# Kernel optimization log

Hardware: AMD Instinct MI355X
Metric: run time of the kernel (lower is better)

Reference implementation:

```python
import jax, jax.numpy as jnp
import numpy as np

HIDDEN = 1024
NUM_HEADS = 16
HEAD_DIM = HIDDEN // NUM_HEADS
EPS = 1e-05


def setup_inputs() -> dict:
    key = jax.random.key(0)
    ks = jax.random.split(key, 6)
    B, S = 4, 2048
    x = jax.random.normal(ks[0], (B, S, HIDDEN), dtype=jnp.float32)
    # trunc_normal_(std=0.02) approximated by scaled normal
    w_in = jax.random.normal(ks[1], (3 * HIDDEN, HIDDEN), dtype=jnp.float32) * 0.02
    b_in = jax.random.normal(ks[2], (3 * HIDDEN,), dtype=jnp.float32) * 0.02
    w_norm = jnp.ones((HIDDEN,), dtype=jnp.float32)
    lim = 1.0 / np.sqrt(HIDDEN)
    w_out = jax.random.uniform(ks[3], (HIDDEN, HIDDEN), dtype=jnp.float32, minval=-lim, maxval=lim)
    b_out = jax.random.uniform(ks[4], (HIDDEN,), dtype=jnp.float32, minval=-lim, maxval=lim)
    return {"x": x, "w_in": w_in, "b_in": b_in, "w_norm": w_norm, "w_out": w_out, "b_out": b_out}


def _rms_norm(x, w, eps):
    var = jnp.mean(jnp.square(x), axis=-1, keepdims=True)
    return x * jax.lax.rsqrt(var + eps) * w


def reference(x, w_in, b_in, w_norm, w_out, b_out):
    B, S, _ = x.shape
    xn = _rms_norm(x, w_norm, EPS)
    qkv = jnp.einsum('bsd,ed->bse', xn, w_in) + b_in  # [B,S,3*HIDDEN]
    q, k, v = jnp.split(qkv, 3, axis=-1)
    # [B,S,H*D] -> [B,H,S,D]
    def split_heads(t):
        return t.reshape(B, S, NUM_HEADS, HEAD_DIM).transpose(0, 2, 1, 3)
    q, k, v = split_heads(q), split_heads(k), split_heads(v)
    scale = 1.0 / np.sqrt(HEAD_DIM)
    scores = jnp.einsum('bhqd,bhkd->bhqk', q, k) * scale
    attn = jax.nn.softmax(scores, axis=-1)
    o = jnp.einsum('bhqk,bhkd->bhqd', attn, v)
    o = o.transpose(0, 2, 1, 3).reshape(B, S, HIDDEN)
    return jnp.einsum('bsd,ed->bse', o, w_out) + b_out
```

## Files before the change

kernel.cpp:

```cpp
#include <hip/hip_runtime.h>
#include <stdint.h>

typedef short bf16x4 __attribute__((ext_vector_type(4)));
typedef short bf16x8 __attribute__((ext_vector_type(8)));
typedef _Float16 f16x8 __attribute__((ext_vector_type(8)));
typedef float f32x4 __attribute__((ext_vector_type(4)));
typedef float f32x16 __attribute__((ext_vector_type(16)));
typedef unsigned int u32x4 __attribute__((ext_vector_type(4)));
typedef unsigned int u32x2 __attribute__((ext_vector_type(2)));

#if __has_builtin(__builtin_amdgcn_exp2f)
#define EXP2 __builtin_amdgcn_exp2f
#else
#define EXP2 exp2f
#endif

__device__ __forceinline__ short f2bf(float f) {
  union { float f; uint32_t u; } v; v.f = f;
  uint32_t r = (v.u + 0x7fffu + ((v.u >> 16) & 1u)) >> 16;
  return (short)(uint16_t)r;
}

__device__ __forceinline__ unsigned cvtpk_bf16(float lo, float hi) {
  unsigned r;
  asm("v_cvt_pk_bf16_f32 %0, %1, %2" : "=v"(r) : "v"(lo), "v"(hi));
  return r;
}

#if __has_builtin(__builtin_amdgcn_permlane32_swap)
__device__ __forceinline__ void plane32_swap(unsigned& a, unsigned& b) {
  u32x2 r = __builtin_amdgcn_permlane32_swap(a, b, false, false);
  a = r[0]; b = r[1];
}
__device__ __forceinline__ float xhalf_max(float x) {
  unsigned xu = __builtin_bit_cast(unsigned, x);
  u32x2 r = __builtin_amdgcn_permlane32_swap(xu, xu, false, false);
  return fmaxf(__builtin_bit_cast(float, r[0]), __builtin_bit_cast(float, r[1]));
}
__device__ __forceinline__ float xhalf_sum(float x) {
  unsigned xu = __builtin_bit_cast(unsigned, x);
  u32x2 r = __builtin_amdgcn_permlane32_swap(xu, xu, false, false);
  return __builtin_bit_cast(float, r[0]) + __builtin_bit_cast(float, r[1]);
}
#else
__device__ __forceinline__ void plane32_swap(unsigned& a, unsigned& b) {
  asm("s_nop 1\n\tv_permlane32_swap_b32 %0, %1" : "+v"(a), "+v"(b));
}
__device__ __forceinline__ float xhalf_max(float x) { return fmaxf(x, __shfl_xor(x, 32, 64)); }
__device__ __forceinline__ float xhalf_sum(float x) { return x + __shfl_xor(x, 32, 64); }
#endif

__device__ __forceinline__ float fmax3(float a, float b, float c) {
  return fmaxf(fmaxf(a, b), c);
}

__device__ __forceinline__ float tmax16(const f32x16& s) {
  float a0 = fmax3(s[0], s[1], s[2]);
  float a1 = fmax3(s[3], s[4], s[5]);
  float a2 = fmax3(s[6], s[7], s[8]);
  float a3 = fmax3(s[9], s[10], s[11]);
  float a4 = fmax3(s[12], s[13], s[14]);
  float b0 = fmax3(a0, a1, s[15]);
  float b1 = fmax3(a2, a3, a4);
  return fmaxf(b0, b1);
}
__device__ __forceinline__ float tsum16(const f32x16& s) {
  float a0 = (s[0] + s[1]) + (s[2] + s[3]);
  float a1 = (s[4] + s[5]) + (s[6] + s[7]);
  float a2 = (s[8] + s[9]) + (s[10] + s[11]);
  float a3 = (s[12] + s[13]) + (s[14] + s[15]);
  return (a0 + a1) + (a2 + a3);
}

__device__ __forceinline__ f32x16 zero16() {
  f32x16 z;
#pragma unroll
  for (int i = 0; i < 16; ++i) z[i] = 0.f;
  return z;
}

__device__ __forceinline__ void gld_lds16(const void* g, void* l) {
  __builtin_amdgcn_global_load_lds(
      (__attribute__((address_space(1))) const void*)g,
      (__attribute__((address_space(3))) void*)l, 16, 0, 0);
}

__global__ __launch_bounds__(256) void k_rmsnorm(const float* __restrict__ x,
                                                 const float* __restrict__ wn,
                                                 short* __restrict__ xn) {
  const int row = blockIdx.x;
  const int t = threadIdx.x;
  const float4 v = reinterpret_cast<const float4*>(x + (size_t)row * 1024)[t];
  float ss = v.x * v.x + v.y * v.y + v.z * v.z + v.w * v.w;
#pragma unroll
  for (int m = 32; m >= 1; m >>= 1) ss += __shfl_xor(ss, m, 64);
  __shared__ float red[4];
  if ((t & 63) == 0) red[t >> 6] = ss;
  __syncthreads();
  const float tot = red[0] + red[1] + red[2] + red[3];
  const float rr = rsqrtf(tot * (1.0f / 1024.0f) + 1e-5f);
  const float4 g = reinterpret_cast<const float4*>(wn)[t];
  bf16x4 o;
  o[0] = f2bf(v.x * rr * g.x);
  o[1] = f2bf(v.y * rr * g.y);
  o[2] = f2bf(v.z * rr * g.z);
  o[3] = f2bf(v.w * rr * g.w);
  reinterpret_cast<bf16x4*>(xn + (size_t)row * 1024)[t] = o;
}

__global__ __launch_bounds__(256) void k_cast_bf(const float* __restrict__ in,
                                                 short* __restrict__ out, int n4) {
  int i = blockIdx.x * 256 + threadIdx.x;
  if (i >= n4) return;
  float4 v = reinterpret_cast<const float4*>(in)[i];
  bf16x4 o;
  o[0] = f2bf(v.x); o[1] = f2bf(v.y); o[2] = f2bf(v.z); o[3] = f2bf(v.w);
  reinterpret_cast<bf16x4*>(out)[i] = o;
}

__global__ __launch_bounds__(256) void k_cast_f16(const float* __restrict__ in,
                                                  _Float16* __restrict__ out, int n4) {
  int i = blockIdx.x * 256 + threadIdx.x;
  if (i >= n4) return;
  float4 v = reinterpret_cast<const float4*>(in)[i];
  _Float16 o[4] = {(_Float16)v.x, (_Float16)v.y, (_Float16)v.z, (_Float16)v.w};
  reinterpret_cast<ulong1*>(out)[i] = *reinterpret_cast<ulong1*>(o);
}

__global__ __launch_bounds__(256) void k_gemm_qkv(const short* __restrict__ A,
                                                  const short* __restrict__ B,
                                                  const float* __restrict__ bias,
                                                  short* __restrict__ qb,
                                                  short* __restrict__ kfrag,
                                                  short* __restrict__ vfrag) {
  __shared__ __align__(16) short As[128 * 32];
  __shared__ __align__(16) short Bs[128 * 32];
  const int t = threadIdx.x;
  const int orig = blockIdx.y * 24 + blockIdx.x;
  const int swz = (orig & 7) * 192 + (orig >> 3);
  const long bn0 = (long)(swz % 24) * 128;
  const long bm0 = (long)(swz / 24) * 128;
  const int w = t >> 6, l = t & 63;
  const int wr = (w >> 1) * 64, wc = (w & 1) * 64;
  const int lm = l & 15, h = l >> 4;
  f32x4 acc[4][4];
#pragma unroll
  for (int i = 0; i < 4; ++i)
#pragma unroll
    for (int j = 0; j < 4; ++j) acc[i][j] = (f32x4){0.f, 0.f, 0.f, 0.f};
  const int srow = t >> 2, scol = (t & 3) * 8;
  const short* Ag = A + (bm0 + srow) * 1024 + scol;
  const short* Bg = B + (bn0 + srow) * 1024 + scol;
  short* AsP = As + t * 8;
  short* BsP = Bs + t * 8;
  for (int kt = 0; kt < 32; ++kt) {
    const int k0 = kt << 5;
    gld_lds16(Ag + k0, AsP);
    gld_lds16(Ag + k0 + 64 * 1024, AsP + 2048);
    gld_lds16(Bg + k0, BsP);
    gld_lds16(Bg + k0 + 64 * 1024, BsP + 2048);
    __syncthreads();
    bf16x8 af[4], bfr[4];
#pragma unroll
    for (int mi = 0; mi < 4; ++mi)
      af[mi] = *reinterpret_cast<const bf16x8*>(As + (wr + mi * 16 + lm) * 32 + h * 8);
#pragma unroll
    for (int ni = 0; ni < 4; ++ni)
      bfr[ni] = *reinterpret_cast<const bf16x8*>(Bs + (wc + ni * 16 + lm) * 32 + h * 8);
    __builtin_amdgcn_s_setprio(1);
#pragma unroll
    for (int mi = 0; mi < 4; ++mi)
#pragma unroll
      for (int ni = 0; ni < 4; ++ni)
        acc[mi][ni] = __builtin_amdgcn_mfma_f32_16x16x32_bf16(af[mi], bfr[ni], acc[mi][ni], 0, 0, 0);
    __builtin_amdgcn_s_setprio(0);
    __syncthreads();
  }
#pragma unroll
  for (int ni = 0; ni < 4; ++ni) {
    const int ncol = (int)bn0 + wc + ni * 16 + lm;
    const float bv = bias[ncol];
    const int which = ncol >> 10;
    const int e = ncol & 1023;
    const int hd = e >> 6, d = e & 63;
#pragma unroll
    for (int mi = 0; mi < 4; ++mi) {
#pragma unroll
      for (int r = 0; r < 4; ++r) {
        const long mrow = bm0 + wr + mi * 16 + h * 4 + r;
        const float val = acc[mi][ni][r] + bv;
        const long bh = (mrow >> 11) * 16 + hd;
        const int seq = (int)(mrow & 2047);
        if (which == 0) {
          const long off = (bh * 2048 + seq) * 64 + d;
          qb[off] = f2bf(val * 0.18033688011112042f);
        } else if (which == 1) {
          const long off = ((bh * 64 + (seq >> 5)) * 4 + (d >> 4)) * 512 +
                           ((seq & 31) | (((d >> 3) & 1) << 5)) * 8 + (d & 7);
          kfrag[off] = f2bf(val);
        } else {
          const long off = (((bh * 64 + (seq >> 5)) * 2 + (d >> 5)) * 2 +
                            ((seq >> 4) & 1)) * 512 +
                           ((d & 31) | (((seq >> 3) & 1) << 5)) * 8 + (seq & 7);
          vfrag[off] = f2bf(val);
        }
      }
    }
  }
}

__global__ __launch_bounds__(256) void k_gemm_out(const _Float16* __restrict__ A,
                                                  const _Float16* __restrict__ B,
                                                  const float* __restrict__ bias,
                                                  float* __restrict__ outp) {
  __shared__ __align__(16) _Float16 As[128 * 32];
  __shared__ __align__(16) _Float16 Bs[128 * 32];
  const int t = threadIdx.x;
  const int orig = blockIdx.y * 8 + blockIdx.x;
  const int swz = (orig & 7) * 64 + (orig >> 3);
  const long bn0 = (long)(swz % 8) * 128;
  const long bm0 = (long)(swz / 8) * 128;
  const int w = t >> 6, l = t & 63;
  const int wr = (w >> 1) * 64, wc = (w & 1) * 64;
  const int lm = l & 15, h = l >> 4;
  f32x4 acc[4][4];
#pragma unroll
  for (int i = 0; i < 4; ++i)
#pragma unroll
    for (int j = 0; j < 4; ++j) acc[i][j] = (f32x4){0.f, 0.f, 0.f, 0.f};
  const int srow = t >> 2, scol = (t & 3) * 8;
  const _Float16* Ag = A + (bm0 + srow) * 1024 + scol;
  const _Float16* Bg = B + (bn0 + srow) * 1024 + scol;
  _Float16* AsP = As + t * 8;
  _Float16* BsP = Bs + t * 8;
  for (int kt = 0; kt < 32; ++kt) {
    const int k0 = kt << 5;
    gld_lds16(Ag + k0, AsP);
    gld_lds16(Ag + k0 + 64 * 1024, AsP + 2048);
    gld_lds16(Bg + k0, BsP);
    gld_lds16(Bg + k0 + 64 * 1024, BsP + 2048);
    __syncthreads();
    f16x8 af[4], bfr[4];
#pragma unroll
    for (int mi = 0; mi < 4; ++mi)
      af[mi] = *reinterpret_cast<const f16x8*>(As + (wr + mi * 16 + lm) * 32 + h * 8);
#pragma unroll
    for (int ni = 0; ni < 4; ++ni)
      bfr[ni] = *reinterpret_cast<const f16x8*>(Bs + (wc + ni * 16 + lm) * 32 + h * 8);
    __builtin_amdgcn_s_setprio(1);
#pragma unroll
    for (int mi = 0; mi < 4; ++mi)
#pragma unroll
      for (int ni = 0; ni < 4; ++ni)
        acc[mi][ni] = __builtin_amdgcn_mfma_f32_16x16x32_f16(af[mi], bfr[ni], acc[mi][ni], 0, 0, 0);
    __builtin_amdgcn_s_setprio(0);
    __syncthreads();
  }
#pragma unroll
  for (int ni = 0; ni < 4; ++ni) {
    const int ncol = (int)bn0 + wc + ni * 16 + lm;
    const float bv = bias[ncol];
#pragma unroll
    for (int mi = 0; mi < 4; ++mi) {
#pragma unroll
      for (int r = 0; r < 4; ++r) {
        const long mrow = bm0 + wr + mi * 16 + h * 4 + r;
        outp[mrow * 1024 + ncol] = acc[mi][ni][r] + bv;
      }
    }
  }
}

__global__ __launch_bounds__(256) void k_attn(const short* __restrict__ q,
                                              const short* __restrict__ kfrag,
                                              const short* __restrict__ vfrag,
                                              _Float16* __restrict__ o) {
  const int orig = blockIdx.y * 8 + blockIdx.x;
  const int work = (orig & 7) * 64 + (orig >> 3);
  const int bh = work >> 3;
  const int qt = work & 7;
  const int t = threadIdx.x;
  const int w = t >> 6, l = t & 63;
  const int lq = l & 31, hh = l >> 5;
  const int qbase = qt * 256 + w * 64;

  bf16x8 qf[2][4];
#pragma unroll
  for (int qh = 0; qh < 2; ++qh) {
    const short* qp = q + ((size_t)(bh * 2048 + qbase + qh * 32 + lq)) * 64 + hh * 8;
#pragma unroll
    for (int db = 0; db < 4; ++db)
      qf[qh][db] = *reinterpret_cast<const bf16x8*>(qp + db * 16);
  }

  const short* kfb = kfrag + (size_t)bh * 64 * 2048 + l * 8;
  const short* vfb = vfrag + (size_t)bh * 64 * 2048 + l * 8;

  f32x16 oa00 = zero16(), oa01 = zero16();
  f32x16 oa10 = zero16(), oa11 = zero16();
  float mr0 = -1e30f, mr1 = -1e30f, lr0 = 0.f, lr1 = 0.f;

  auto LOAD = [&](bf16x8* kf, bf16x8* vf, int kt) {
    const short* kp = kfb + (size_t)kt * 2048;
#pragma unroll
    for (int db = 0; db < 4; ++db)
      kf[db] = *reinterpret_cast<const bf16x8*>(kp + db * 512);
    const short* vp = vfb + (size_t)kt * 2048;
#pragma unroll
    for (int i = 0; i < 4; ++i)
      vf[i] = *reinterpret_cast<const bf16x8*>(vp + i * 512);
  };

  auto COMPUTE = [&](const bf16x8* kf, const bf16x8* vf) {
    f32x16 s0 = zero16(), s1 = zero16();
    __builtin_amdgcn_s_setprio(1);
#pragma unroll
    for (int db = 0; db < 4; ++db) {
      s0 = __builtin_amdgcn_mfma_f32_32x32x16_bf16(kf[db], qf[0][db], s0, 0, 0, 0);
      s1 = __builtin_amdgcn_mfma_f32_32x32x16_bf16(kf[db], qf[1][db], s1, 0, 0, 0);
    }
    __builtin_amdgcn_s_setprio(0);
    float tm0 = xhalf_max(tmax16(s0));
    float tm1 = xhalf_max(tmax16(s1));
    if (!__all((tm0 <= mr0 + 8.f) && (tm1 <= mr1 + 8.f))) {
      const float mn0 = fmaxf(mr0, tm0), mn1 = fmaxf(mr1, tm1);
      const float c0 = EXP2(mr0 - mn0), c1 = EXP2(mr1 - mn1);
      lr0 *= c0; lr1 *= c1;
#pragma unroll
      for (int r = 0; r < 16; ++r) {
        oa00[r] *= c0; oa01[r] *= c0;
        oa10[r] *= c1; oa11[r] *= c1;
      }
      mr0 = mn0; mr1 = mn1;
    }
#pragma unroll
    for (int r = 0; r < 16; ++r) {
      s0[r] = EXP2(s0[r] - mr0);
      s1[r] = EXP2(s1[r] - mr1);
    }
    lr0 += tsum16(s0);
    lr1 += tsum16(s1);
    __builtin_amdgcn_s_setprio(1);
#pragma unroll
    for (int kg = 0; kg < 2; ++kg) {
      const int b0 = kg * 8;
      unsigned p00 = cvtpk_bf16(s0[b0 + 0], s0[b0 + 1]);
      unsigned p01 = cvtpk_bf16(s0[b0 + 2], s0[b0 + 3]);
      unsigned p02 = cvtpk_bf16(s0[b0 + 4], s0[b0 + 5]);
      unsigned p03 = cvtpk_bf16(s0[b0 + 6], s0[b0 + 7]);
      plane32_swap(p00, p02);
      plane32_swap(p01, p03);
      u32x4 pw0 = {p00, p01, p02, p03};
      bf16x8 pf0 = *reinterpret_cast<bf16x8*>(&pw0);
      unsigned p10 = cvtpk_bf16(s1[b0 + 0], s1[b0 + 1]);
      unsigned p11 = cvtpk_bf16(s1[b0 + 2], s1[b0 + 3]);
      unsigned p12 = cvtpk_bf16(s1[b0 + 4], s1[b0 + 5]);
      unsigned p13 = cvtpk_bf16(s1[b0 + 6], s1[b0 + 7]);
      plane32_swap(p10, p12);
      plane32_swap(p11, p13);
      u32x4 pw1 = {p10, p11, p12, p13};
      bf16x8 pf1 = *reinterpret_cast<bf16x8*>(&pw1);
      oa00 = __builtin_amdgcn_mfma_f32_32x32x16_bf16(vf[0 * 2 + kg], pf0, oa00, 0, 0, 0);
      oa10 = __builtin_amdgcn_mfma_f32_32x32x16_bf16(vf[0 * 2 + kg], pf1, oa10, 0, 0, 0);
      oa01 = __builtin_amdgcn_mfma_f32_32x32x16_bf16(vf[1 * 2 + kg], pf0, oa01, 0, 0, 0);
      oa11 = __builtin_amdgcn_mfma_f32_32x32x16_bf16(vf[1 * 2 + kg], pf1, oa11, 0, 0, 0);
    }
    __builtin_amdgcn_s_setprio(0);
  };

  bf16x8 kfA[4], vfA[4], kfB[4], vfB[4];
  LOAD(kfA, vfA, 0);
  for (int kt = 0; kt < 64; kt += 2) {
    LOAD(kfB, vfB, kt + 1);
    COMPUTE(kfA, vfA);
    int k2 = kt + 2; if (k2 > 63) k2 = 63;
    LOAD(kfA, vfA, k2);
    COMPUTE(kfB, vfB);
  }
  const float inv0 = 1.0f / xhalf_sum(lr0);
  const float inv1 = 1.0f / xhalf_sum(lr1);
  const int b = bh >> 4, hd = bh & 15;
  _Float16* ob0 = o + ((size_t)(b * 2048 + qbase + lq)) * 1024 + hd * 64;
  _Float16* ob1 = ob0 + 32 * 1024;
#pragma unroll
  for (int r2 = 0; r2 < 16; ++r2) {
    const int d0 = (r2 & 3) + 8 * (r2 >> 2) + 4 * hh;
    ob0[d0] = (_Float16)(oa00[r2] * inv0);
    ob0[d0 + 32] = (_Float16)(oa01[r2] * inv0);
    ob1[d0] = (_Float16)(oa10[r2] * inv1);
    ob1[d0 + 32] = (_Float16)(oa11[r2] * inv1);
  }
}

extern "C" void kernel_launch(void* const* d_in, const int* in_sizes, int n_in,
                              void* d_out, int out_size, void* d_ws, size_t ws_size,
                              hipStream_t stream) {
  const float* x = (const float*)d_in[0];
  const float* w_in = (const float*)d_in[1];
  const float* b_in = (const float*)d_in[2];
  const float* w_norm = (const float*)d_in[3];
  const float* w_out = (const float*)d_in[4];
  const float* b_out = (const float*)d_in[5];
  float* out = (float*)d_out;
  char* ws = (char*)d_ws;
  short* xn = (short*)(ws);
  short* win_b = (short*)(ws + 16777216);
  _Float16* wout_h = (_Float16*)(ws + 23068672);
  short* qb = (short*)(ws + 25165824);
  short* kfrag = (short*)(ws + 41943040);
  short* vfrag = (short*)(ws + 58720256);
  _Float16* ob = (_Float16*)(ws + 75497472);

  k_cast_bf<<<3072, 256, 0, stream>>>(w_in, win_b, 786432);
  k_cast_f16<<<1024, 256, 0, stream>>>(w_out, wout_h, 262144);
  k_rmsnorm<<<8192, 256, 0, stream>>>(x, w_norm, xn);
  k_gemm_qkv<<<dim3(24, 64), 256, 0, stream>>>(xn, win_b, b_in, qb, kfrag, vfrag);
  k_attn<<<dim3(8, 64), 256, 0, stream>>>(qb, kfrag, vfrag, ob);
  k_gemm_out<<<dim3(8, 64), 256, 0, stream>>>(ob, wout_h, b_out, out);
}
```

Baseline: 232.6 us.

## Split attention KV range in two halves and merge partial outputs

Splits each attention work item across two blocks that each process half of the key tiles. Each block writes normalized partial outputs plus per-row max and sum statistics, and a new merge kernel combines them with log-sum-exp weights. This doubles the attention grid to raise CU occupancy and parallelism. In exchange it adds an extra kernel launch and about 48MB of extra fp16 read/write traffic for the merge.

```diff
diff --git a/kernel.cpp b/kernel.cpp
--- a/kernel.cpp
+++ b/kernel.cpp
@@ -3,6 +3,7 @@
 
 typedef short bf16x4 __attribute__((ext_vector_type(4)));
 typedef short bf16x8 __attribute__((ext_vector_type(8)));
+typedef _Float16 f16x4 __attribute__((ext_vector_type(4)));
 typedef _Float16 f16x8 __attribute__((ext_vector_type(8)));
 typedef float f32x4 __attribute__((ext_vector_type(4)));
 typedef float f32x16 __attribute__((ext_vector_type(16)));
@@ -274,11 +275,14 @@
 __global__ __launch_bounds__(256) void k_attn(const short* __restrict__ q,
                                               const short* __restrict__ kfrag,
                                               const short* __restrict__ vfrag,
-                                              _Float16* __restrict__ o) {
-  const int orig = blockIdx.y * 8 + blockIdx.x;
-  const int work = (orig & 7) * 64 + (orig >> 3);
-  const int bh = work >> 3;
-  const int qt = work & 7;
+                                              _Float16* __restrict__ po0,
+                                              _Float16* __restrict__ po1,
+                                              float* __restrict__ stats) {
+  const int orig = blockIdx.y * 16 + blockIdx.x;
+  const int work = (orig & 7) * 128 + (orig >> 3);
+  const int bh = work >> 4;
+  const int qt = (work >> 1) & 7;
+  const int half = work & 1;
   const int t = threadIdx.x;
   const int w = t >> 6, l = t & 63;
   const int lq = l & 31, hh = l >> 5;
@@ -369,18 +373,22 @@
   };
 
   bf16x8 kfA[4], vfA[4], kfB[4], vfB[4];
-  LOAD(kfA, vfA, 0);
-  for (int kt = 0; kt < 64; kt += 2) {
+  const int kt0 = half * 32, kt1 = kt0 + 32;
+  LOAD(kfA, vfA, kt0);
+  for (int kt = kt0; kt < kt1; kt += 2) {
     LOAD(kfB, vfB, kt + 1);
     COMPUTE(kfA, vfA);
-    int k2 = kt + 2; if (k2 > 63) k2 = 63;
+    int k2 = kt + 2; if (k2 >= kt1) k2 = kt1 - 1;
     LOAD(kfA, vfA, k2);
     COMPUTE(kfB, vfB);
   }
-  const float inv0 = 1.0f / xhalf_sum(lr0);
-  const float inv1 = 1.0f / xhalf_sum(lr1);
+  const float lt0 = xhalf_sum(lr0);
+  const float lt1 = xhalf_sum(lr1);
+  const float inv0 = 1.0f / lt0;
+  const float inv1 = 1.0f / lt1;
   const int b = bh >> 4, hd = bh & 15;
-  _Float16* ob0 = o + ((size_t)(b * 2048 + qbase + lq)) * 1024 + hd * 64;
+  _Float16* po = half ? po1 : po0;
+  _Float16* ob0 = po + ((size_t)(b * 2048 + qbase + lq)) * 1024 + hd * 64;
   _Float16* ob1 = ob0 + 32 * 1024;
 #pragma unroll
   for (int r2 = 0; r2 < 16; ++r2) {
@@ -390,6 +398,39 @@
     ob1[d0] = (_Float16)(oa10[r2] * inv1);
     ob1[d0 + 32] = (_Float16)(oa11[r2] * inv1);
   }
+  if (hh == 0) {
+    float* st = stats + (size_t)half * 262144;
+    const size_t si = (size_t)bh * 2048 + qbase + lq;
+    st[si] = mr0;
+    st[131072 + si] = lt0;
+    st[si + 32] = mr1;
+    st[131072 + si + 32] = lt1;
+  }
+}
+
+__global__ __launch_bounds__(256) void k_merge(_Float16* __restrict__ po0,
+                                               const _Float16* __restrict__ po1,
+                                               const float* __restrict__ stats) {
+  const int row = blockIdx.x;
+  const int t = threadIdx.x;
+  const int col = t * 4;
+  const int hd = col >> 6;
+  const int b = row >> 11, s = row & 2047;
+  const size_t si = (size_t)(b * 16 + hd) * 2048 + s;
+  const float m0 = stats[si], l0 = stats[131072 + si];
+  const float m1 = stats[262144 + si], l1 = stats[393216 + si];
+  const float mm = fmaxf(m0, m1);
+  const float w0 = l0 * EXP2(m0 - mm), w1 = l1 * EXP2(m1 - mm);
+  const float inv = 1.0f / (w0 + w1);
+  const float a0 = w0 * inv, a1 = w1 * inv;
+  const size_t off = (size_t)row * 1024 + col;
+  f16x4 v0 = *reinterpret_cast<const f16x4*>(po0 + off);
+  f16x4 v1 = *reinterpret_cast<const f16x4*>(po1 + off);
+  f16x4 r;
+#pragma unroll
+  for (int j = 0; j < 4; ++j)
+    r[j] = (_Float16)(a0 * (float)v0[j] + a1 * (float)v1[j]);
+  *reinterpret_cast<f16x4*>(po0 + off) = r;
 }
 
 extern "C" void kernel_launch(void* const* d_in, const int* in_sizes, int n_in,
@@ -404,17 +445,20 @@
   float* out = (float*)d_out;
   char* ws = (char*)d_ws;
   short* xn = (short*)(ws);
+  _Float16* po1 = (_Float16*)(ws);
   short* win_b = (short*)(ws + 16777216);
+  float* stats = (float*)(ws + 16777216);
   _Float16* wout_h = (_Float16*)(ws + 23068672);
   short* qb = (short*)(ws + 25165824);
   short* kfrag = (short*)(ws + 41943040);
   short* vfrag = (short*)(ws + 58720256);
-  _Float16* ob = (_Float16*)(ws + 75497472);
+  _Float16* po0 = (_Float16*)(ws + 75497472);
 
   k_cast_bf<<<3072, 256, 0, stream>>>(w_in, win_b, 786432);
   k_cast_f16<<<1024, 256, 0, stream>>>(w_out, wout_h, 262144);
   k_rmsnorm<<<8192, 256, 0, stream>>>(x, w_norm, xn);
   k_gemm_qkv<<<dim3(24, 64), 256, 0, stream>>>(xn, win_b, b_in, qb, kfrag, vfrag);
-  k_attn<<<dim3(8, 64), 256, 0, stream>>>(qb, kfrag, vfrag, ob);
-  k_gemm_out<<<dim3(8, 64), 256, 0, stream>>>(ob, wout_h, b_out, out);
-}
+  k_attn<<<dim3(16, 64), 256, 0, stream>>>(qb, kfrag, vfrag, po0, po1, stats);
+  k_merge<<<8192, 256, 0, stream>>>(po0, po1, stats);
+  k_gemm_out<<<dim3(8, 64), 256, 0, stream>>>(po0, wout_h, b_out, out);
+}
```

Result: slower. 252.0 us (+8.4%).

## Halve per-wave query rows in attention to raise occupancy

Applied to the files above, without the earlier changes.

Each wave now handles 32 query rows instead of 64, so per-thread accumulators and Q fragments are halved, and the grid doubles to 1024 blocks with launch bounds requesting 4 blocks per CU. V fragments are no longer double-buffered and are loaded just before each compute step. The aim is more waves and better latency hiding. In exchange, K/V are read from global memory twice as often per query row, and each K/V fragment feeds fewer MFMAs.

```diff
diff --git a/kernel.cpp b/kernel.cpp
--- a/kernel.cpp
+++ b/kernel.cpp
@@ -271,40 +271,38 @@
   }
 }
 
-__global__ __launch_bounds__(256) void k_attn(const short* __restrict__ q,
-                                              const short* __restrict__ kfrag,
-                                              const short* __restrict__ vfrag,
-                                              _Float16* __restrict__ o) {
-  const int orig = blockIdx.y * 8 + blockIdx.x;
-  const int work = (orig & 7) * 64 + (orig >> 3);
-  const int bh = work >> 3;
-  const int qt = work & 7;
+__global__ __launch_bounds__(256, 4) void k_attn(const short* __restrict__ q,
+                                                 const short* __restrict__ kfrag,
+                                                 const short* __restrict__ vfrag,
+                                                 _Float16* __restrict__ o) {
+  const int orig = blockIdx.y * 16 + blockIdx.x;
+  const int work = (orig & 7) * 128 + (orig >> 3);
+  const int bh = work >> 4;
+  const int qt = work & 15;
   const int t = threadIdx.x;
   const int w = t >> 6, l = t & 63;
   const int lq = l & 31, hh = l >> 5;
-  const int qbase = qt * 256 + w * 64;
-
-  bf16x8 qf[2][4];
-#pragma unroll
-  for (int qh = 0; qh < 2; ++qh) {
-    const short* qp = q + ((size_t)(bh * 2048 + qbase + qh * 32 + lq)) * 64 + hh * 8;
-#pragma unroll
-    for (int db = 0; db < 4; ++db)
-      qf[qh][db] = *reinterpret_cast<const bf16x8*>(qp + db * 16);
-  }
+  const int qrow = qt * 128 + w * 32 + lq;
+
+  bf16x8 qf[4];
+  const short* qp = q + ((size_t)(bh * 2048 + qrow)) * 64 + hh * 8;
+#pragma unroll
+  for (int db = 0; db < 4; ++db)
+    qf[db] = *reinterpret_cast<const bf16x8*>(qp + db * 16);
 
   const short* kfb = kfrag + (size_t)bh * 64 * 2048 + l * 8;
   const short* vfb = vfrag + (size_t)bh * 64 * 2048 + l * 8;
 
-  f32x16 oa00 = zero16(), oa01 = zero16();
-  f32x16 oa10 = zero16(), oa11 = zero16();
-  float mr0 = -1e30f, mr1 = -1e30f, lr0 = 0.f, lr1 = 0.f;
-
-  auto LOAD = [&](bf16x8* kf, bf16x8* vf, int kt) {
+  f32x16 oa0 = zero16(), oa1 = zero16();
+  float mr = -1e30f, lr = 0.f;
+
+  auto LOADK = [&](bf16x8* kf, int kt) {
     const short* kp = kfb + (size_t)kt * 2048;
 #pragma unroll
     for (int db = 0; db < 4; ++db)
       kf[db] = *reinterpret_cast<const bf16x8*>(kp + db * 512);
+  };
+  auto LOADV = [&](bf16x8* vf, int kt) {
     const short* vp = vfb + (size_t)kt * 2048;
 #pragma unroll
     for (int i = 0; i < 4; ++i)
@@ -312,83 +310,61 @@
   };
 
   auto COMPUTE = [&](const bf16x8* kf, const bf16x8* vf) {
-    f32x16 s0 = zero16(), s1 = zero16();
+    f32x16 s = zero16();
     __builtin_amdgcn_s_setprio(1);
 #pragma unroll
-    for (int db = 0; db < 4; ++db) {
-      s0 = __builtin_amdgcn_mfma_f32_32x32x16_bf16(kf[db], qf[0][db], s0, 0, 0, 0);
-      s1 = __builtin_amdgcn_mfma_f32_32x32x16_bf16(kf[db], qf[1][db], s1, 0, 0, 0);
+    for (int db = 0; db < 4; ++db)
+      s = __builtin_amdgcn_mfma_f32_32x32x16_bf16(kf[db], qf[db], s, 0, 0, 0);
+    __builtin_amdgcn_s_setprio(0);
+    float tm = xhalf_max(tmax16(s));
+    if (!__all(tm <= mr + 8.f)) {
+      const float mn = fmaxf(mr, tm);
+      const float c = EXP2(mr - mn);
+      lr *= c;
+#pragma unroll
+      for (int r = 0; r < 16; ++r) { oa0[r] *= c; oa1[r] *= c; }
+      mr = mn;
     }
-    __builtin_amdgcn_s_setprio(0);
-    float tm0 = xhalf_max(tmax16(s0));
-    float tm1 = xhalf_max(tmax16(s1));
-    if (!__all((tm0 <= mr0 + 8.f) && (tm1 <= mr1 + 8.f))) {
-      const float mn0 = fmaxf(mr0, tm0), mn1 = fmaxf(mr1, tm1);
-      const float c0 = EXP2(mr0 - mn0), c1 = EXP2(mr1 - mn1);
-      lr0 *= c0; lr1 *= c1;
-#pragma unroll
-      for (int r = 0; r < 16; ++r) {
-        oa00[r] *= c0; oa01[r] *= c0;
-        oa10[r] *= c1; oa11[r] *= c1;
-      }
-      mr0 = mn0; mr1 = mn1;
-    }
-#pragma unroll
-    for (int r = 0; r < 16; ++r) {
-      s0[r] = EXP2(s0[r] - mr0);
-      s1[r] = EXP2(s1[r] - mr1);
-    }
-    lr0 += tsum16(s0);
-    lr1 += tsum16(s1);
+#pragma unroll
+    for (int r = 0; r < 16; ++r) s[r] = EXP2(s[r] - mr);
+    lr += tsum16(s);
     __builtin_amdgcn_s_setprio(1);
 #pragma unroll
     for (int kg = 0; kg < 2; ++kg) {
       const int b0 = kg * 8;
-      unsigned p00 = cvtpk_bf16(s0[b0 + 0], s0[b0 + 1]);
-      unsigned p01 = cvtpk_bf16(s0[b0 + 2], s0[b0 + 3]);
-      unsigned p02 = cvtpk_bf16(s0[b0 + 4], s0[b0 + 5]);
-      unsigned p03 = cvtpk_bf16(s0[b0 + 6], s0[b0 + 7]);
-      plane32_swap(p00, p02);
-      plane32_swap(p01, p03);
-      u32x4 pw0 = {p00, p01, p02, p03};
-      bf16x8 pf0 = *reinterpret_cast<bf16x8*>(&pw0);
-      unsigned p10 = cvtpk_bf16(s1[b0 + 0], s1[b0 + 1]);
-      unsigned p11 = cvtpk_bf16(s1[b0 + 2], s1[b0 + 3]);
-      unsigned p12 = cvtpk_bf16(s1[b0 + 4], s1[b0 + 5]);
-      unsigned p13 = cvtpk_bf16(s1[b0 + 6], s1[b0 + 7]);
-      plane32_swap(p10, p12);
-      plane32_swap(p11, p13);
-      u32x4 pw1 = {p10, p11, p12, p13};
-      bf16x8 pf1 = *reinterpret_cast<bf16x8*>(&pw1);
-      oa00 = __builtin_amdgcn_mfma_f32_32x32x16_bf16(vf[0 * 2 + kg], pf0, oa00, 0, 0, 0);
-      oa10 = __builtin_amdgcn_mfma_f32_32x32x16_bf16(vf[0 * 2 + kg], pf1, oa10, 0, 0, 0);
-      oa01 = __builtin_amdgcn_mfma_f32_32x32x16_bf16(vf[1 * 2 + kg], pf0, oa01, 0, 0, 0);
-      oa11 = __builtin_amdgcn_mfma_f32_32x32x16_bf16(vf[1 * 2 + kg], pf1, oa11, 0, 0, 0);
+      unsigned w0 = cvtpk_bf16(s[b0 + 0], s[b0 + 1]);
+      unsigned w1 = cvtpk_bf16(s[b0 + 2], s[b0 + 3]);
+      unsigned w2 = cvtpk_bf16(s[b0 + 4], s[b0 + 5]);
+      unsigned w3 = cvtpk_bf16(s[b0 + 6], s[b0 + 7]);
+      plane32_swap(w0, w2);
+      plane32_swap(w1, w3);
+      u32x4 pw = {w0, w1, w2, w3};
+      bf16x8 pf = *reinterpret_cast<bf16x8*>(&pw);
+      oa0 = __builtin_amdgcn_mfma_f32_32x32x16_bf16(vf[0 * 2 + kg], pf, oa0, 0, 0, 0);
+      oa1 = __builtin_amdgcn_mfma_f32_32x32x16_bf16(vf[1 * 2 + kg], pf, oa1, 0, 0, 0);
     }
     __builtin_amdgcn_s_setprio(0);
   };
 
-  bf16x8 kfA[4], vfA[4], kfB[4], vfB[4];
-  LOAD(kfA, vfA, 0);
+  bf16x8 kfA[4], kfB[4], vf[4];
+  LOADK(kfA, 0);
   for (int kt = 0; kt < 64; kt += 2) {
-    LOAD(kfB, vfB, kt + 1);
-    COMPUTE(kfA, vfA);
+    LOADK(kfB, kt + 1);
+    LOADV(vf, kt);
+    COMPUTE(kfA, vf);
     int k2 = kt + 2; if (k2 > 63) k2 = 63;
-    LOAD(kfA, vfA, k2);
-    COMPUTE(kfB, vfB);
-  }
-  const float inv0 = 1.0f / xhalf_sum(lr0);
-  const float inv1 = 1.0f / xhalf_sum(lr1);
+    LOADK(kfA, k2);
+    LOADV(vf, kt + 1);
+    COMPUTE(kfB, vf);
+  }
+  const float inv = 1.0f / xhalf_sum(lr);
   const int b = bh >> 4, hd = bh & 15;
-  _Float16* ob0 = o + ((size_t)(b * 2048 + qbase + lq)) * 1024 + hd * 64;
-  _Float16* ob1 = ob0 + 32 * 1024;
+  _Float16* ob = o + ((size_t)(b * 2048 + qrow)) * 1024 + hd * 64;
 #pragma unroll
   for (int r2 = 0; r2 < 16; ++r2) {
     const int d0 = (r2 & 3) + 8 * (r2 >> 2) + 4 * hh;
-    ob0[d0] = (_Float16)(oa00[r2] * inv0);
-    ob0[d0 + 32] = (_Float16)(oa01[r2] * inv0);
-    ob1[d0] = (_Float16)(oa10[r2] * inv1);
-    ob1[d0 + 32] = (_Float16)(oa11[r2] * inv1);
+    ob[d0] = (_Float16)(oa0[r2] * inv);
+    ob[d0 + 32] = (_Float16)(oa1[r2] * inv);
   }
 }
 
@@ -415,6 +391,6 @@
   k_cast_f16<<<1024, 256, 0, stream>>>(w_out, wout_h, 262144);
   k_rmsnorm<<<8192, 256, 0, stream>>>(x, w_norm, xn);
   k_gemm_qkv<<<dim3(24, 64), 256, 0, stream>>>(xn, win_b, b_in, qb, kfrag, vfrag);
-  k_attn<<<dim3(8, 64), 256, 0, stream>>>(qb, kfrag, vfrag, ob);
+  k_attn<<<dim3(16, 64), 256, 0, stream>>>(qb, kfrag, vfrag, ob);
   k_gemm_out<<<dim3(8, 64), 256, 0, stream>>>(ob, wout_h, b_out, out);
 }
```

Result: faster. 226.8 us (-2.5%).
